# Performance work log

Hardware: AMD Instinct MI355X
Metric: run time of the kernel (lower is better)

## Reference

```python
import jax, jax.numpy as jnp
import numpy as np

M, I, J = 524288, 16, 16


def setup_inputs() -> dict:
    key = jax.random.key(0)
    k1, k2, k3, k4 = jax.random.split(key, 4)
    h = jax.random.normal(k1, (2, 1, 1, I, J), dtype=jnp.float32)
    gi = jax.random.normal(k2, (2, M, 1, I), dtype=jnp.float32)
    gj = jax.random.normal(k3, (2, 1, M, J), dtype=jnp.float32)
    theta = jax.random.uniform(k4, (2, M), dtype=jnp.float32) * (2.0 * np.pi)
    return {"h": h, "gi": gi, "gj": gj, "theta": theta}


def reference(h, gi, gj, theta):
    # Theta = diag(cos(theta[0])) + 1j * diag(sin(theta[1])) -- diagonal, so the
    # per-(i,j) bilinear form gj_j @ Theta @ gi_i is an O(M) contraction.
    tre = jnp.cos(theta[0])  # [M]
    tim = jnp.sin(theta[1])  # [M]
    a, b = gj[0, 0], gj[1, 0]            # [M, J] real/imag of gj
    e, f = gi[0, :, 0, :], gi[1, :, 0, :]  # [M, I] real/imag of gi
    # u = Theta_diag * gj (complex elementwise along M)
    u_re = a * tre[:, None] - b * tim[:, None]  # [M, J]
    u_im = a * tim[:, None] + b * tre[:, None]  # [M, J]
    # out[i,j] = sum_m gi[m,i] * theta[m] * gj[m,j] (complex)
    out_re = jnp.einsum('mi,mj->ij', e, u_re) - jnp.einsum('mi,mj->ij', f, u_im)
    out_im = jnp.einsum('mi,mj->ij', e, u_im) + jnp.einsum('mi,mj->ij', f, u_re)
    # htilde = h + reflected path, then squeeze the singleton dims -> [2, I, J]
    return h[:, 0, 0] + jnp.stack([out_re, out_im], axis=0)
```

## Files before the change

### kernel.cpp

```cpp
#include <hip/hip_runtime.h>


constexpr int MDIM    = 524288;
constexpr int THREADS = 256;
constexpr int BLOCKS  = 1024;
constexpr int M_PER_B = MDIM / BLOCKS;
constexpr int CHUNK   = 64;
constexpr int NCHUNK  = M_PER_B / CHUNK;
constexpr int T0_OFF  = 4096;
constexpr int T1_OFF  = 4160;
constexpr int BUF_F   = 4224;

typedef float f32x2 __attribute__((ext_vector_type(2)));

#define AS1 __attribute__((address_space(1)))
#define AS3 __attribute__((address_space(3)))

__device__ __forceinline__ void cp16(const float* g, float* l) {
    __builtin_amdgcn_global_load_lds((const AS1 void*)g, (AS3 void*)l, 16, 0, 0);
}
__device__ __forceinline__ void cp4(const float* g, float* l) {
    __builtin_amdgcn_global_load_lds((const AS1 void*)g, (AS3 void*)l, 4, 0, 0);
}

__device__ __forceinline__ void stage_chunk(
    const float* __restrict__ gi, const float* __restrict__ gj,
    const float* __restrict__ theta, float* buf, int m0, int wave, int lane)
{
    const float* gsrc;
    if      (wave == 0) gsrc = gi + (size_t)m0 * 16;
    else if (wave == 1) gsrc = gi + (size_t)MDIM * 16 + (size_t)m0 * 16;
    else if (wave == 2) gsrc = gj + (size_t)m0 * 16;
    else                gsrc = gj + (size_t)MDIM * 16 + (size_t)m0 * 16;
    float* ldst = buf + wave * 1024;
#pragma unroll
    for (int j = 0; j < 4; ++j) {
        cp16(gsrc + j * 256 + lane * 4, ldst + j * 256);
    }
    if (wave == 0) {
        cp4(theta + m0 + lane,        buf + T0_OFF);
        cp4(theta + MDIM + m0 + lane, buf + T1_OFF);
    }
}

__device__ __forceinline__ void compute_chunk(
    const float* buf, int slot, int i0, int j0,
    f32x2 (&are)[4][2], f32x2 (&aim)[4][2])
{
#pragma unroll
    for (int k = 0; k < 4; ++k) {
        const int ml = slot + 16 * k;
        const float4 e4 = *(const float4*)(buf +        ml * 16 + i0);
        const float4 f4 = *(const float4*)(buf + 1024 + ml * 16 + i0);
        const float4 a4 = *(const float4*)(buf + 2048 + ml * 16 + j0);
        const float4 b4 = *(const float4*)(buf + 3072 + ml * 16 + j0);
        const float c = __cosf(buf[T0_OFF + ml]);
        const float s = __sinf(buf[T1_OFF + ml]);
        const f32x2 cc = {c, c}, ss = {s, s};
        const f32x2 a01 = {a4.x, a4.y}, a23 = {a4.z, a4.w};
        const f32x2 b01 = {b4.x, b4.y}, b23 = {b4.z, b4.w};
        f32x2 ure[2], uim[2];
        ure[0] = __builtin_elementwise_fma(-b01, ss, a01 * cc);
        ure[1] = __builtin_elementwise_fma(-b23, ss, a23 * cc);
        uim[0] = __builtin_elementwise_fma( b01, cc, a01 * ss);
        uim[1] = __builtin_elementwise_fma( b23, cc, a23 * ss);
        const float ev[4] = {e4.x, e4.y, e4.z, e4.w};
        const float fv[4] = {f4.x, f4.y, f4.z, f4.w};
#pragma unroll
        for (int i = 0; i < 4; ++i) {
            const f32x2 ee = {ev[i], ev[i]};
            const f32x2 ff = {fv[i], fv[i]};
#pragma unroll
            for (int jp = 0; jp < 2; ++jp) {
                are[i][jp] = __builtin_elementwise_fma( ee, ure[jp], are[i][jp]);
                are[i][jp] = __builtin_elementwise_fma(-ff, uim[jp], are[i][jp]);
                aim[i][jp] = __builtin_elementwise_fma( ee, uim[jp], aim[i][jp]);
                aim[i][jp] = __builtin_elementwise_fma( ff, ure[jp], aim[i][jp]);
            }
        }
    }
}

template <bool USE_ATOMIC>
__device__ __forceinline__ void theta_body(
    const float* __restrict__ gi, const float* __restrict__ gj,
    const float* __restrict__ theta, float* __restrict__ dst)
{
    __shared__ float smem[2 * BUF_F];
    const int t    = threadIdx.x;
    const int wave = t >> 6;
    const int lane = t & 63;
    const int slot = t >> 4;
    const int tile = t & 15;
    const int i0   = (tile >> 2) << 2;
    const int j0   = (tile & 3) << 2;
    const int m_base = blockIdx.x * M_PER_B;

    f32x2 are[4][2], aim[4][2];
#pragma unroll
    for (int i = 0; i < 4; ++i)
#pragma unroll
        for (int jp = 0; jp < 2; ++jp) { are[i][jp] = {0.f, 0.f}; aim[i][jp] = {0.f, 0.f}; }

    stage_chunk(gi, gj, theta, smem, m_base, wave, lane);
    for (int c = 0; c < NCHUNK; ++c) {
        __syncthreads();
        if (c + 1 < NCHUNK)
            stage_chunk(gi, gj, theta, smem + ((c + 1) & 1) * BUF_F,
                        m_base + (c + 1) * CHUNK, wave, lane);
        compute_chunk(smem + (c & 1) * BUF_F, slot & 3 ? slot : slot, i0, j0, are, aim);
    }

    float sre[4][4], sim[4][4];
#pragma unroll
    for (int i = 0; i < 4; ++i)
#pragma unroll
        for (int jp = 0; jp < 2; ++jp) {
            sre[i][jp * 2]     = are[i][jp].x;  sre[i][jp * 2 + 1] = are[i][jp].y;
            sim[i][jp * 2]     = aim[i][jp].x;  sim[i][jp * 2 + 1] = aim[i][jp].y;
        }

#pragma unroll
    for (int i = 0; i < 4; ++i)
#pragma unroll
        for (int j = 0; j < 4; ++j) {
            sre[i][j] += __shfl_xor(sre[i][j], 16);
            sre[i][j] += __shfl_xor(sre[i][j], 32);
            sim[i][j] += __shfl_xor(sim[i][j], 16);
            sim[i][j] += __shfl_xor(sim[i][j], 32);
        }

    float (*red)[16][33] = (float (*)[16][33])smem;
    if (lane < 16) {
#pragma unroll
        for (int i = 0; i < 4; ++i)
#pragma unroll
            for (int j = 0; j < 4; ++j) {
                red[wave][lane][i * 4 + j]      = sre[i][j];
                red[wave][lane][16 + i * 4 + j] = sim[i][j];
            }
    }
    __syncthreads();

#pragma unroll
    for (int k = 0; k < 2; ++k) {
        const int idx = t * 2 + k;
        const int tl  = idx >> 5;
        const int v   = idx & 31;
        const float sum = red[0][tl][v] + red[1][tl][v] + red[2][tl][v] + red[3][tl][v];
        const int ii  = ((tl >> 2) << 2) + ((v & 15) >> 2);
        const int jj  = ((tl & 3) << 2) + (v & 3);
        const int off = ((v & 16) ? 256 : 0) + ii * 16 + jj;
        if (USE_ATOMIC) atomicAdd(dst + off, sum);
        else            dst[blockIdx.x * 512 + off] = sum;
    }
}

__global__ __launch_bounds__(THREADS, 4) void theta_main_ws(
    const float* __restrict__ gi, const float* __restrict__ gj,
    const float* __restrict__ theta, float* __restrict__ partial)
{
    theta_body<false>(gi, gj, theta, partial);
}

__global__ __launch_bounds__(THREADS, 4) void theta_main_atomic(
    const float* __restrict__ gi, const float* __restrict__ gj,
    const float* __restrict__ theta, float* __restrict__ out)
{
    theta_body<true>(gi, gj, theta, out);
}

__global__ __launch_bounds__(256) void theta_reduce(
    const float* __restrict__ h, const float* __restrict__ partial,
    float* __restrict__ out)
{
    const int w    = (blockIdx.x * 256 + threadIdx.x) >> 6;
    const int lane = threadIdx.x & 63;
    float s = 0.f;
#pragma unroll 4
    for (int j = 0; j < BLOCKS / 64; ++j)
        s += partial[(size_t)(j * 64 + lane) * 512 + w];
#pragma unroll
    for (int d = 1; d < 64; d <<= 1) s += __shfl_xor(s, d);
    if (lane == 0) out[w] = h[w] + s;
}

__global__ void theta_init(const float* __restrict__ h, float* __restrict__ out) {
    int k = blockIdx.x * blockDim.x + threadIdx.x;
    if (k < 512) out[k] = h[k];
}

extern "C" void kernel_launch(void* const* d_in, const int* in_sizes, int n_in,
                              void* d_out, int out_size, void* d_ws, size_t ws_size,
                              hipStream_t stream) {
    const float* h     = (const float*)d_in[0];
    const float* gi    = (const float*)d_in[1];
    const float* gj    = (const float*)d_in[2];
    const float* theta = (const float*)d_in[3];
    float* out = (float*)d_out;

    const size_t need = (size_t)BLOCKS * 512 * sizeof(float);
    if (ws_size >= need) {
        float* partial = (float*)d_ws;
        theta_main_ws<<<BLOCKS, THREADS, 0, stream>>>(gi, gj, theta, partial);
        theta_reduce<<<128, 256, 0, stream>>>(h, partial, out);
    } else {
        theta_init<<<2, 256, 0, stream>>>(h, out);
        theta_main_atomic<<<BLOCKS, THREADS, 0, stream>>>(gi, gj, theta, out);
    }
}
```

Before: 163.4 us.

## Give each wave its own M range with a three-deep async LDS pipeline

Each of the four waves now streams its own slice of M through a private triple-buffered LDS region of 16-row chunks. Completion is tracked with explicit s_waitcnt vmcnt counts, so the per-chunk __syncthreads is gone. The grid is halved to 512 blocks and the launch-bounds occupancy hint is removed. This aims to keep more global loads in flight and cut block-wide barrier stalls. In exchange, LDS per block is larger, so fewer blocks fit per CU, and correctness now depends on hand-counted vmcnt values matching the number of issued loads.

Measured after the change: 161.0 us. No clear change (-1.5%).

```diff
diff --git a/kernel.cpp b/kernel.cpp
--- a/kernel.cpp
+++ b/kernel.cpp
@@ -3,13 +3,19 @@
 
 constexpr int MDIM    = 524288;
 constexpr int THREADS = 256;
-constexpr int BLOCKS  = 1024;
+constexpr int BLOCKS  = 512;
 constexpr int M_PER_B = MDIM / BLOCKS;
-constexpr int CHUNK   = 64;
-constexpr int NCHUNK  = M_PER_B / CHUNK;
-constexpr int T0_OFF  = 4096;
-constexpr int T1_OFF  = 4160;
-constexpr int BUF_F   = 4224;
+constexpr int M_PER_W = M_PER_B / 4;
+constexpr int CHUNK   = 16;
+constexpr int NCH     = M_PER_W / CHUNK;
+constexpr int DEPTH   = 3;
+
+constexpr int E_OFF = 0, F_OFF = 256, A_OFF = 512, B_OFF = 768;
+constexpr int T0_OFF = 1024, T1_OFF = 1040;
+constexpr int BUF_F  = 1056;
+constexpr int WAVE_F = DEPTH * BUF_F;
+constexpr int SMEM_F = 4 * WAVE_F;
+static_assert(SMEM_F * sizeof(float) <= 65536, "LDS must stay under 64 KiB");
 
 typedef float f32x2 __attribute__((ext_vector_type(2)));
 
@@ -23,23 +29,18 @@
     __builtin_amdgcn_global_load_lds((const AS1 void*)g, (AS3 void*)l, 4, 0, 0);
 }
 
-__device__ __forceinline__ void stage_chunk(
-    const float* __restrict__ gi, const float* __restrict__ gj,
-    const float* __restrict__ theta, float* buf, int m0, int wave, int lane)
-{
-    const float* gsrc;
-    if      (wave == 0) gsrc = gi + (size_t)m0 * 16;
-    else if (wave == 1) gsrc = gi + (size_t)MDIM * 16 + (size_t)m0 * 16;
-    else if (wave == 2) gsrc = gj + (size_t)m0 * 16;
-    else                gsrc = gj + (size_t)MDIM * 16 + (size_t)m0 * 16;
-    float* ldst = buf + wave * 1024;
-#pragma unroll
-    for (int j = 0; j < 4; ++j) {
-        cp16(gsrc + j * 256 + lane * 4, ldst + j * 256);
-    }
-    if (wave == 0) {
-        cp4(theta + m0 + lane,        buf + T0_OFF);
-        cp4(theta + MDIM + m0 + lane, buf + T1_OFF);
+__device__ __forceinline__ void stage(
+    const float* e_g, const float* f_g, const float* a_g, const float* b_g,
+    const float* t0_g, const float* t1_g, float* buf, int p, int lane)
+{
+    const size_t mo = (size_t)p * (CHUNK * 16);
+    cp16(e_g + mo, buf + E_OFF);
+    cp16(f_g + mo, buf + F_OFF);
+    cp16(a_g + mo, buf + A_OFF);
+    cp16(b_g + mo, buf + B_OFF);
+    if (lane < 16) {
+        cp4(t0_g + (size_t)p * CHUNK, buf + T0_OFF);
+        cp4(t1_g + (size_t)p * CHUNK, buf + T1_OFF);
     }
 }
 
@@ -49,11 +50,11 @@
 {
 #pragma unroll
     for (int k = 0; k < 4; ++k) {
-        const int ml = slot + 16 * k;
-        const float4 e4 = *(const float4*)(buf +        ml * 16 + i0);
-        const float4 f4 = *(const float4*)(buf + 1024 + ml * 16 + i0);
-        const float4 a4 = *(const float4*)(buf + 2048 + ml * 16 + j0);
-        const float4 b4 = *(const float4*)(buf + 3072 + ml * 16 + j0);
+        const int ml = slot + 4 * k;
+        const float4 e4 = *(const float4*)(buf + E_OFF + ml * 16 + i0);
+        const float4 f4 = *(const float4*)(buf + F_OFF + ml * 16 + i0);
+        const float4 a4 = *(const float4*)(buf + A_OFF + ml * 16 + j0);
+        const float4 b4 = *(const float4*)(buf + B_OFF + ml * 16 + j0);
         const float c = __cosf(buf[T0_OFF + ml]);
         const float s = __sinf(buf[T1_OFF + ml]);
         const f32x2 cc = {c, c}, ss = {s, s};
@@ -86,15 +87,23 @@
     const float* __restrict__ gi, const float* __restrict__ gj,
     const float* __restrict__ theta, float* __restrict__ dst)
 {
-    __shared__ float smem[2 * BUF_F];
+    __shared__ float smem[SMEM_F];
     const int t    = threadIdx.x;
     const int wave = t >> 6;
     const int lane = t & 63;
-    const int slot = t >> 4;
-    const int tile = t & 15;
+    const int slot = (lane >> 4) & 3;
+    const int tile = lane & 15;
     const int i0   = (tile >> 2) << 2;
     const int j0   = (tile & 3) << 2;
-    const int m_base = blockIdx.x * M_PER_B;
+    const int m_w0 = blockIdx.x * M_PER_B + wave * M_PER_W;
+    float* wbase   = smem + wave * WAVE_F;
+
+    const float* e_g  = gi + (size_t)m_w0 * 16 + lane * 4;
+    const float* f_g  = e_g + (size_t)MDIM * 16;
+    const float* a_g  = gj + (size_t)m_w0 * 16 + lane * 4;
+    const float* b_g  = a_g + (size_t)MDIM * 16;
+    const float* t0_g = theta + m_w0 + lane;
+    const float* t1_g = t0_g + MDIM;
 
     f32x2 are[4][2], aim[4][2];
 #pragma unroll
@@ -102,14 +111,22 @@
 #pragma unroll
         for (int jp = 0; jp < 2; ++jp) { are[i][jp] = {0.f, 0.f}; aim[i][jp] = {0.f, 0.f}; }
 
-    stage_chunk(gi, gj, theta, smem, m_base, wave, lane);
-    for (int c = 0; c < NCHUNK; ++c) {
-        __syncthreads();
-        if (c + 1 < NCHUNK)
-            stage_chunk(gi, gj, theta, smem + ((c + 1) & 1) * BUF_F,
-                        m_base + (c + 1) * CHUNK, wave, lane);
-        compute_chunk(smem + (c & 1) * BUF_F, slot & 3 ? slot : slot, i0, j0, are, aim);
-    }
+    stage(e_g, f_g, a_g, b_g, t0_g, t1_g, wbase + 0 * BUF_F, 0, lane);
+    stage(e_g, f_g, a_g, b_g, t0_g, t1_g, wbase + 1 * BUF_F, 1, lane);
+
+    int sb = 2, cb = 0;
+    for (int c = 0; c < NCH - 2; ++c) {
+        stage(e_g, f_g, a_g, b_g, t0_g, t1_g, wbase + sb * BUF_F, c + 2, lane);
+        sb = (sb == DEPTH - 1) ? 0 : sb + 1;
+        asm volatile("s_waitcnt vmcnt(12)" ::: "memory");
+        compute_chunk(wbase + cb * BUF_F, slot, i0, j0, are, aim);
+        cb = (cb == DEPTH - 1) ? 0 : cb + 1;
+    }
+    asm volatile("s_waitcnt vmcnt(6)" ::: "memory");
+    compute_chunk(wbase + cb * BUF_F, slot, i0, j0, are, aim);
+    cb = (cb == DEPTH - 1) ? 0 : cb + 1;
+    asm volatile("s_waitcnt vmcnt(0)" ::: "memory");
+    compute_chunk(wbase + cb * BUF_F, slot, i0, j0, are, aim);
 
     float sre[4][4], sim[4][4];
 #pragma unroll
@@ -130,6 +147,7 @@
             sim[i][j] += __shfl_xor(sim[i][j], 32);
         }
 
+    __syncthreads();
     float (*red)[16][33] = (float (*)[16][33])smem;
     if (lane < 16) {
 #pragma unroll
@@ -156,14 +174,14 @@
     }
 }
 
-__global__ __launch_bounds__(THREADS, 4) void theta_main_ws(
+__global__ __launch_bounds__(THREADS) void theta_main_ws(
     const float* __restrict__ gi, const float* __restrict__ gj,
     const float* __restrict__ theta, float* __restrict__ partial)
 {
     theta_body<false>(gi, gj, theta, partial);
 }
 
-__global__ __launch_bounds__(THREADS, 4) void theta_main_atomic(
+__global__ __launch_bounds__(THREADS) void theta_main_atomic(
     const float* __restrict__ gi, const float* __restrict__ gj,
     const float* __restrict__ theta, float* __restrict__ out)
 {
```
